# Performance work log

Measured on AMD Instinct MI355X. Metric: run time of the kernel, lower is better.

The kernel has to match this reference:

```python
import jax, jax.numpy as jnp
import numpy as np
import math

EMBED_DIM = 256
N_HEAD = 8
N_LEVELS = 4
N_POINTS = 4
HEAD_DIM = EMBED_DIM // N_HEAD
TOTAL_POINTS = N_HEAD * N_LEVELS * N_POINTS
SPATIAL = np.array([[100, 100], [50, 50], [25, 25], [13, 13]], dtype=np.int32)
BS = 2
LEN_Q = int(SPATIAL.prod(1).sum())  # 13294, encoder self-attention
LEN_V = LEN_Q


def setup_inputs() -> dict:
    key = jax.random.key(0)
    ks = jax.random.split(key, 12)
    s = 1.0 / math.sqrt(EMBED_DIM)
    inp = {
        'query': jax.random.normal(ks[0], (BS, LEN_Q, EMBED_DIM), jnp.float32),
        'reference_points': jax.random.uniform(ks[1], (BS, LEN_Q, N_LEVELS, 2), jnp.float32),
        'value': jax.random.normal(ks[2], (BS, LEN_V, EMBED_DIM), jnp.float32),
        'value_spatial_shapes': jnp.asarray(SPATIAL),
        'W_value': jax.random.normal(ks[3], (EMBED_DIM, EMBED_DIM), jnp.float32) * s,
        'b_value': jnp.zeros((EMBED_DIM,), jnp.float32),
        'W_off': jax.random.normal(ks[4], (TOTAL_POINTS * 2, EMBED_DIM), jnp.float32) * 0.01,
        'b_off': jax.random.normal(ks[5], (TOTAL_POINTS * 2,), jnp.float32),
        'W_attn': jax.random.normal(ks[6], (TOTAL_POINTS, EMBED_DIM), jnp.float32) * s,
        'b_attn': jnp.zeros((TOTAL_POINTS,), jnp.float32),
        'W_out': jax.random.normal(ks[7], (EMBED_DIM, EMBED_DIM), jnp.float32) * s,
        'b_out': jnp.zeros((EMBED_DIM,), jnp.float32),
        'zeta': jnp.ones((1, 1, 1, HEAD_DIM), jnp.float32),  # search_type='embed'
    }
    return inp


def _grid_sample_bilinear(img, gx, gy):
    """img: [B,H,W,c]; gx,gy: [B,Q,P] normalized to [-1,1].
    align_corners=False, padding_mode='zeros' (matches F.grid_sample)."""
    B, H, W, c = img.shape
    x = (gx + 1.0) * (0.5 * W) - 0.5
    y = (gy + 1.0) * (0.5 * H) - 0.5
    x0 = jnp.floor(x)
    y0 = jnp.floor(y)
    wx = (x - x0)[..., None]
    wy = (y - y0)[..., None]
    flat = img.reshape(B, H * W, c)

    def gather(xi, yi):
        m = (xi >= 0) & (xi < W) & (yi >= 0) & (yi < H)
        xi_c = jnp.clip(xi, 0, W - 1).astype(jnp.int32)
        yi_c = jnp.clip(yi, 0, H - 1).astype(jnp.int32)
        idx = (yi_c * W + xi_c).reshape(B, -1, 1)
        v = jnp.take_along_axis(flat, idx, axis=1).reshape(B, *xi.shape[1:], c)
        return v * m[..., None]

    v00 = gather(x0, y0)
    v01 = gather(x0 + 1, y0)
    v10 = gather(x0, y0 + 1)
    v11 = gather(x0 + 1, y0 + 1)
    return (v00 * (1 - wx) * (1 - wy) + v01 * wx * (1 - wy)
            + v10 * (1 - wx) * wy + v11 * wx * wy)


def reference(query, reference_points, value, value_spatial_shapes,
              W_value, b_value, W_off, b_off, W_attn, b_attn, W_out, b_out, zeta):
    bs, Len_q, _ = query.shape
    Len_v = value.shape[1]
    shapes = np.asarray(value_spatial_shapes)  # static ints

    # value projection + sparse gate (zeta, not pruned/searched)
    v = value @ W_value.T + b_value
    v = v.reshape(bs, Len_v, N_HEAD, HEAD_DIM) * zeta  # [bs,Lv,h,c]

    # sampling offsets and attention weights from query
    off = (query @ W_off.T + b_off).reshape(bs, Len_q, N_HEAD, N_LEVELS, N_POINTS, 2)
    attn = (query @ W_attn.T + b_attn).reshape(bs, Len_q, N_HEAD, N_LEVELS * N_POINTS)
    attn = jax.nn.softmax(attn, axis=-1).reshape(bs, Len_q, N_HEAD, N_LEVELS, N_POINTS)

    # reference_points last dim == 2 branch
    normalizer = jnp.asarray(shapes[:, ::-1], jnp.float32).reshape(1, 1, 1, N_LEVELS, 1, 2)  # (W,H)
    loc = reference_points.reshape(bs, Len_q, 1, N_LEVELS, 1, 2) + off / normalizer
    grids = 2.0 * loc - 1.0  # [bs,Lq,h,L,P,2]

    B = bs * N_HEAD
    out = jnp.zeros((B, Len_q, HEAD_DIM), jnp.float32)
    start = 0
    for lvl in range(N_LEVELS):
        h, w = int(shapes[lvl, 0]), int(shapes[lvl, 1])
        # [bs, h*w, nh, c] -> [bs*nh, h, w, c]
        v_l = v[:, start:start + h * w].transpose(0, 2, 1, 3).reshape(B, h, w, HEAD_DIM)
        g = grids[:, :, :, lvl].transpose(0, 2, 1, 3, 4).reshape(B, Len_q, N_POINTS, 2)
        samp = _grid_sample_bilinear(v_l, g[..., 0], g[..., 1])  # [B,Lq,P,c]
        a_l = attn[:, :, :, lvl].transpose(0, 2, 1, 3).reshape(B, Len_q, N_POINTS)
        out = out + jnp.einsum('bqpc,bqp->bqc', samp, a_l)
        start += h * w

    out = out.reshape(bs, N_HEAD, Len_q, HEAD_DIM).transpose(0, 2, 1, 3).reshape(bs, Len_q, EMBED_DIM)
    return out @ W_out.T + b_out
```

## Files before the change

### kernel.cpp

```cpp
#include <hip/hip_runtime.h>


#define LQ    13294
#define NTOK  26588
#define NE    6806528

typedef unsigned short ushort_t;
typedef __attribute__((ext_vector_type(8))) short short8;
typedef __attribute__((ext_vector_type(8))) unsigned short ushort8_t;
typedef __attribute__((ext_vector_type(4))) float float4_t;

__device__ __forceinline__ ushort_t f2b(float f) {
    unsigned int x = __float_as_uint(f);
    return (ushort_t)((x + 0x7fffu + ((x >> 16) & 1u)) >> 16);
}

__device__ __forceinline__ void gload16(const void* g, void* l) {
    __builtin_amdgcn_global_load_lds(
        (const __attribute__((address_space(1))) unsigned int*)g,
        (__attribute__((address_space(3))) unsigned int*)l, 16, 0, 0);
}

__device__ __forceinline__ void cvt_seg(const float* __restrict__ s,
                                        ushort_t* __restrict__ d,
                                        int n4, int gid, int stride) {
    const float4_t* s4 = (const float4_t*)s;
    for (int i = gid; i < n4; i += stride) {
        float4_t f = s4[i];
        ushort4 o;
        o.x = f2b(f.x); o.y = f2b(f.y); o.z = f2b(f.z); o.w = f2b(f.w);
        *(ushort4*)(d + (long)i * 4) = o;
    }
}

__global__ __launch_bounds__(256) void cvt_k(
    const float* q, const float* v, const float* Wv, const float* Wo,
    const float* Wa, const float* Wout,
    ushort_t* q_bf, ushort_t* v_bf, ushort_t* Wv_bf, ushort_t* WoWa_bf,
    ushort_t* Wout_bf)
{
    const int gid = blockIdx.x * 256 + threadIdx.x;
    const int stride = gridDim.x * 256;
    cvt_seg(q,    q_bf,            NE / 4,     gid, stride);
    cvt_seg(v,    v_bf,            NE / 4,     gid, stride);
    cvt_seg(Wv,   Wv_bf,           65536 / 4,  gid, stride);
    cvt_seg(Wo,   WoWa_bf,         65536 / 4,  gid, stride);
    cvt_seg(Wa,   WoWa_bf + 65536, 32768 / 4,  gid, stride);
    cvt_seg(Wout, Wout_bf,         65536 / 4,  gid, stride);
}

__device__ __forceinline__ void gemm_tile(
    const ushort_t* __restrict__ A,
    const ushort_t* __restrict__ W,
    int m0, int n0,
    ushort_t* As, ushort_t* Bs, float4_t acc[2][4])
{
    const int tid = threadIdx.x;
    const int w  = tid >> 6;
    const int ln = tid & 63;
    const int lr = ln >> 2;
    const int lc = (ln & 3) * 8;

    ushort_t* lA0 = As + (w * 2 + 0) * 512;
    ushort_t* lA1 = As + (w * 2 + 1) * 512;
    ushort_t* lB  = Bs + w * 512;
    const ushort_t* gA0 = A + (long)(m0 + w * 32 + lr) * 256 + lc;
    const ushort_t* gA1 = gA0 + 16 * 256;
    const ushort_t* gB  = W + (long)(n0 + w * 16 + lr) * 256 + lc;

    const int krow = (ln >> 4) * 8;
    const int fr   = ln & 15;

    gload16(gA0, lA0);
    gload16(gA1, lA1);
    gload16(gB,  lB);
    __syncthreads();

    #pragma unroll
    for (int kt = 0; kt < 8; kt++) {
        const int cur = kt & 1;
        if (kt < 7) {
            const int nxt = cur ^ 1;
            gload16(gA0 + (kt + 1) * 32, lA0 + nxt * 4096);
            gload16(gA1 + (kt + 1) * 32, lA1 + nxt * 4096);
            gload16(gB  + (kt + 1) * 32, lB  + nxt * 2048);
        }
        short8 af[2], bfr[4];
        #pragma unroll
        for (int i = 0; i < 2; i++)
            af[i] = *(const short8*)(As + cur * 4096 + (w * 32 + i * 16 + fr) * 32 + krow);
        #pragma unroll
        for (int j = 0; j < 4; j++)
            bfr[j] = *(const short8*)(Bs + cur * 2048 + (j * 16 + fr) * 32 + krow);
        #pragma unroll
        for (int i = 0; i < 2; i++)
            #pragma unroll
            for (int j = 0; j < 4; j++)
                acc[i][j] = __builtin_amdgcn_mfma_f32_16x16x32_bf16(af[i], bfr[j], acc[i][j], 0, 0, 0);
        __syncthreads();
    }
}

__global__ __launch_bounds__(256) void gemm_fused_k(
    const ushort_t* __restrict__ q_bf, const ushort_t* __restrict__ v_bf,
    const ushort_t* __restrict__ Wv,   const ushort_t* __restrict__ WoWa,
    const float* __restrict__ b_value, const float* __restrict__ b_off,
    const float* __restrict__ b_attn,  const float* __restrict__ zeta,
    ushort_t* __restrict__ vproj, float* __restrict__ oa)
{
    __shared__ __align__(16) ushort_t As[2 * 4096];
    __shared__ __align__(16) ushort_t Bs[2 * 2048];

    const int z = blockIdx.z;
    const int bid = blockIdx.x;
    int x, y;
    if (z == 0) {
        if (bid >= 832) return;
        int id = (bid & 7) * 104 + (bid >> 3);
        x = id >> 2; y = id & 3;
    } else {
        int id = (bid & 7) * 156 + (bid >> 3);
        x = id / 6; y = id - x * 6;
    }
    const int m0 = x * 128;
    const int n0 = y * 64;

    float4_t acc[2][4] = {};
    gemm_tile(z ? q_bf : v_bf, z ? WoWa : Wv, m0, n0, As, Bs, acc);

    const int tid = threadIdx.x;
    const int w = tid >> 6, ln = tid & 63;
    const int col = ln & 15;
    const int rq  = (ln >> 4) * 4;
    #pragma unroll
    for (int j = 0; j < 4; j++) {
        int n = n0 + j * 16 + col;
        if (z == 0) {
            float bz = b_value[n];
            float zz = zeta[n & 31];
            long hbase = (long)(n >> 5) * NTOK;
            #pragma unroll
            for (int i = 0; i < 2; i++) {
                #pragma unroll
                for (int r = 0; r < 4; r++) {
                    int m = m0 + w * 32 + i * 16 + rq + r;
                    if (m < NTOK)
                        vproj[(hbase + m) * 32 + (n & 31)] = f2b((acc[i][j][r] + bz) * zz);
                }
            }
        } else {
            float bz = (n < 256) ? b_off[n] : b_attn[n - 256];
            #pragma unroll
            for (int i = 0; i < 2; i++) {
                #pragma unroll
                for (int r = 0; r < 4; r++) {
                    int m = m0 + w * 32 + i * 16 + rq + r;
                    if (m < NTOK) oa[(long)m * 384 + n] = acc[i][j][r] + bz;
                }
            }
        }
    }
}

__global__ __launch_bounds__(256) void gemm_out_k(
    const ushort_t* __restrict__ A,
    const ushort_t* __restrict__ W,
    const float* __restrict__ bias,
    float* __restrict__ C)
{
    __shared__ __align__(16) ushort_t As[2 * 4096];
    __shared__ __align__(16) ushort_t Bs[2 * 2048];

    const int bid = blockIdx.x;
    int id = (bid & 7) * 104 + (bid >> 3);
    const int m0 = (id >> 2) * 128;
    const int n0 = (id & 3) * 64;

    float4_t acc[2][4] = {};
    gemm_tile(A, W, m0, n0, As, Bs, acc);

    const int tid = threadIdx.x;
    const int w = tid >> 6, ln = tid & 63;
    const int col = ln & 15;
    const int rq  = (ln >> 4) * 4;
    #pragma unroll
    for (int j = 0; j < 4; j++) {
        int n = n0 + j * 16 + col;
        float bz = bias[n];
        #pragma unroll
        for (int i = 0; i < 2; i++) {
            #pragma unroll
            for (int r = 0; r < 4; r++) {
                int m = m0 + w * 32 + i * 16 + rq + r;
                if (m < NTOK) C[(long)m * 256 + n] = acc[i][j][r] + bz;
            }
        }
    }
}

__global__ __launch_bounds__(512, 8) void sample_k(
    const float* __restrict__ refp,
    const ushort_t* __restrict__ v,
    const float* __restrict__ oa,
    ushort_t* __restrict__ outp)
{
    __shared__ __align__(16) int   p_ofs[576][4];
    __shared__ __align__(16) float p_w[576][4];
    const int bid = blockIdx.x;
    const int h   = bid & 7;
    const int tbase = (bid >> 3) * 32;
    const int tid = threadIdx.x;

    {
        const int tok1 = tid >> 4, p = tid & 15;
        const long t = tbase + tok1;
        if (t < NTOK) {
            const int lvl = p >> 2;
            const int Wi  = (lvl == 0) ? 100 : (lvl == 1) ? 50 : (lvl == 2) ? 25 : 13;
            const int st  = (lvl == 0) ? 0 : (lvl == 1) ? 10000 : (lvl == 2) ? 12500 : 13125;
            const float Wf = (float)Wi;
            const int b = (t >= LQ) ? 1 : 0;

            float lg = oa[t * 384 + 256 + h * 16 + p];
            float smax = lg;
            #pragma unroll
            for (int d = 1; d < 16; d <<= 1) smax = fmaxf(smax, __shfl_xor(smax, d, 64));
            float ex = __expf(lg - smax);
            float sm = ex;
            #pragma unroll
            for (int d = 1; d < 16; d <<= 1) sm += __shfl_xor(sm, d, 64);
            const float a = ex / sm;

            float ox = oa[t * 384 + h * 32 + p * 2];
            float oy = oa[t * 384 + h * 32 + p * 2 + 1];
            float rx = refp[t * 8 + lvl * 2];
            float ry = refp[t * 8 + lvl * 2 + 1];

            float x = rx * Wf + ox - 0.5f;
            float y = ry * Wf + oy - 0.5f;
            float xf = floorf(x), yf = floorf(y);
            float wx = x - xf, wy = y - yf;
            int x0 = (int)xf, y0 = (int)yf;

            float mx0 = ((unsigned)x0       < (unsigned)Wi) ? (1.f - wx) : 0.f;
            float mx1 = ((unsigned)(x0 + 1) < (unsigned)Wi) ? wx         : 0.f;
            float my0 = ((unsigned)y0       < (unsigned)Wi) ? (1.f - wy) * a : 0.f;
            float my1 = ((unsigned)(y0 + 1) < (unsigned)Wi) ? wy * a         : 0.f;
            int x0c = min(max(x0, 0), Wi - 1);
            int x1c = min(max(x0 + 1, 0), Wi - 1);
            int y0c = min(max(y0, 0), Wi - 1);
            int y1c = min(max(y0 + 1, 0), Wi - 1);

            const int hb = h * NTOK + b * LQ + st;
            const int r0 = hb + y0c * Wi, r1 = hb + y1c * Wi;
            const int su = tid + (tid >> 3);
            p_ofs[su][0] = (r0 + x0c) << 6;
            p_ofs[su][1] = (r0 + x1c) << 6;
            p_ofs[su][2] = (r1 + x0c) << 6;
            p_ofs[su][3] = (r1 + x1c) << 6;
            p_w[su][0] = mx0 * my0;
            p_w[su][1] = mx1 * my0;
            p_w[su][2] = mx0 * my1;
            p_w[su][3] = mx1 * my1;
        }
    }
    __syncthreads();

    const int tok2 = tid >> 4, l16 = tid & 15, s = l16 >> 2, g = l16 & 3;
    const long t = tbase + tok2;
    if (t < NTOK) {
        const char* vb = (const char*)v;
        const unsigned go = g * 16;
        const int ub = tok2 * 16 + s * 4;
        float4_t accA = {0.f, 0.f, 0.f, 0.f};
        float4_t accB = {0.f, 0.f, 0.f, 0.f};

        #pragma unroll 2
        for (int q = 0; q < 4; q++) {
            const int u = ub + q;
            const int su = u + (u >> 3);
            int4     o  = *(const int4*)p_ofs[su];
            float4_t w4 = *(const float4_t*)p_w[su];
            uint4 u00 = *(const uint4*)(vb + (unsigned)(o.x + go));
            uint4 u01 = *(const uint4*)(vb + (unsigned)(o.y + go));
            uint4 u10 = *(const uint4*)(vb + (unsigned)(o.z + go));
            uint4 u11 = *(const uint4*)(vb + (unsigned)(o.w + go));
            #define ACC8(U, WGT) \
                accA[0] += (WGT) * __uint_as_float((U).x << 16); \
                accA[1] += (WGT) * __uint_as_float((U).x & 0xffff0000u); \
                accA[2] += (WGT) * __uint_as_float((U).y << 16); \
                accA[3] += (WGT) * __uint_as_float((U).y & 0xffff0000u); \
                accB[0] += (WGT) * __uint_as_float((U).z << 16); \
                accB[1] += (WGT) * __uint_as_float((U).z & 0xffff0000u); \
                accB[2] += (WGT) * __uint_as_float((U).w << 16); \
                accB[3] += (WGT) * __uint_as_float((U).w & 0xffff0000u);
            ACC8(u00, w4.x)
            ACC8(u01, w4.y)
            ACC8(u10, w4.z)
            ACC8(u11, w4.w)
            #undef ACC8
        }

        #pragma unroll
        for (int c = 0; c < 4; c++) {
            accA[c] += __shfl_down(accA[c], 8, 64);
            accB[c] += __shfl_down(accB[c], 8, 64);
        }
        #pragma unroll
        for (int c = 0; c < 4; c++) {
            accA[c] += __shfl_down(accA[c], 4, 64);
            accB[c] += __shfl_down(accB[c], 4, 64);
        }

        if (s == 0) {
            ushort8_t o8;
            o8[0] = f2b(accA[0]); o8[1] = f2b(accA[1]);
            o8[2] = f2b(accA[2]); o8[3] = f2b(accA[3]);
            o8[4] = f2b(accB[0]); o8[5] = f2b(accB[1]);
            o8[6] = f2b(accB[2]); o8[7] = f2b(accB[3]);
            *(ushort8_t*)(outp + t * 256 + h * 32 + g * 8) = o8;
        }
    }
}

extern "C" void kernel_launch(void* const* d_in, const int* in_sizes, int n_in,
                              void* d_out, int out_size, void* d_ws, size_t ws_size,
                              hipStream_t stream)
{
    char* ws = (char*)d_ws;
    ushort_t* vproj   = (ushort_t*)ws;
    float*    oa      = (float*)(ws + (long)NE * 2);
    ushort_t* q_bf    = (ushort_t*)(ws + (long)NE * 2 + (long)NTOK * 1536);
    ushort_t* outpre  = q_bf;
    ushort_t* v_bf    = q_bf + NE;
    ushort_t* Wv_bf   = v_bf + NE;
    ushort_t* WoWa_bf = Wv_bf + 65536;
    ushort_t* Wout_bf = WoWa_bf + 98304;

    cvt_k<<<2048, 256, 0, stream>>>(
        (const float*)d_in[0], (const float*)d_in[2], (const float*)d_in[4],
        (const float*)d_in[6], (const float*)d_in[8], (const float*)d_in[10],
        q_bf, v_bf, Wv_bf, WoWa_bf, Wout_bf);

    gemm_fused_k<<<dim3(1248, 1, 2), 256, 0, stream>>>(
        q_bf, v_bf, Wv_bf, WoWa_bf,
        (const float*)d_in[5], (const float*)d_in[7], (const float*)d_in[9],
        (const float*)d_in[12], vproj, oa);

    sample_k<<<8 * 831, 512, 0, stream>>>(
        (const float*)d_in[1], vproj, oa, outpre);

    gemm_out_k<<<832, 256, 0, stream>>>(
        outpre, Wout_bf, (const float*)d_in[11], (float*)d_out);
}
```

Measured before the change: 202.5 us.

## Load GEMM A fragments directly from global, stage full W tile in LDS once

The shared GEMM tile no longer double-buffers A and W through LDS with a barrier every K step. The entire 64x256 W slice is now loaded into LDS once up front, and each wave reads its A fragments directly from global memory into registers. This removes seven per-iteration barriers and the LDS round trip for A. In exchange, A global loads are strided and less coalesced, LDS per block grows to 32KB, and launch bounds now request 4 blocks per CU.

```diff
diff --git a/kernel.cpp b/kernel.cpp
--- a/kernel.cpp
+++ b/kernel.cpp
@@ -53,63 +53,52 @@
     const ushort_t* __restrict__ A,
     const ushort_t* __restrict__ W,
     int m0, int n0,
-    ushort_t* As, ushort_t* Bs, float4_t acc[2][4])
+    ushort_t* Bs, float4_t acc[2][4])
 {
     const int tid = threadIdx.x;
     const int w  = tid >> 6;
     const int ln = tid & 63;
-    const int lr = ln >> 2;
-    const int lc = (ln & 3) * 8;
-
-    ushort_t* lA0 = As + (w * 2 + 0) * 512;
-    ushort_t* lA1 = As + (w * 2 + 1) * 512;
-    ushort_t* lB  = Bs + w * 512;
-    const ushort_t* gA0 = A + (long)(m0 + w * 32 + lr) * 256 + lc;
-    const ushort_t* gA1 = gA0 + 16 * 256;
-    const ushort_t* gB  = W + (long)(n0 + w * 16 + lr) * 256 + lc;
+
+    {
+        const int br = tid >> 2;
+        const int bc = (tid & 3) * 8;
+        const ushort_t* gB = W + (long)(n0 + br) * 256 + bc;
+        ushort_t* lB = Bs + tid * 8;
+        #pragma unroll
+        for (int r = 0; r < 8; r++)
+            gload16(gB + r * 32, lB + r * 2048);
+    }
+    __syncthreads();
 
     const int krow = (ln >> 4) * 8;
     const int fr   = ln & 15;
-
-    gload16(gA0, lA0);
-    gload16(gA1, lA1);
-    gload16(gB,  lB);
-    __syncthreads();
+    const ushort_t* gA0 = A + (long)(m0 + w * 32 + fr) * 256 + krow;
+    const ushort_t* gA1 = gA0 + 16 * 256;
 
     #pragma unroll
     for (int kt = 0; kt < 8; kt++) {
-        const int cur = kt & 1;
-        if (kt < 7) {
-            const int nxt = cur ^ 1;
-            gload16(gA0 + (kt + 1) * 32, lA0 + nxt * 4096);
-            gload16(gA1 + (kt + 1) * 32, lA1 + nxt * 4096);
-            gload16(gB  + (kt + 1) * 32, lB  + nxt * 2048);
-        }
         short8 af[2], bfr[4];
-        #pragma unroll
-        for (int i = 0; i < 2; i++)
-            af[i] = *(const short8*)(As + cur * 4096 + (w * 32 + i * 16 + fr) * 32 + krow);
+        af[0] = *(const short8*)(gA0 + kt * 32);
+        af[1] = *(const short8*)(gA1 + kt * 32);
         #pragma unroll
         for (int j = 0; j < 4; j++)
-            bfr[j] = *(const short8*)(Bs + cur * 2048 + (j * 16 + fr) * 32 + krow);
+            bfr[j] = *(const short8*)(Bs + kt * 2048 + (j * 16 + fr) * 32 + krow);
         #pragma unroll
         for (int i = 0; i < 2; i++)
             #pragma unroll
             for (int j = 0; j < 4; j++)
                 acc[i][j] = __builtin_amdgcn_mfma_f32_16x16x32_bf16(af[i], bfr[j], acc[i][j], 0, 0, 0);
-        __syncthreads();
-    }
-}
-
-__global__ __launch_bounds__(256) void gemm_fused_k(
+    }
+}
+
+__global__ __launch_bounds__(256, 4) void gemm_fused_k(
     const ushort_t* __restrict__ q_bf, const ushort_t* __restrict__ v_bf,
     const ushort_t* __restrict__ Wv,   const ushort_t* __restrict__ WoWa,
     const float* __restrict__ b_value, const float* __restrict__ b_off,
     const float* __restrict__ b_attn,  const float* __restrict__ zeta,
     ushort_t* __restrict__ vproj, float* __restrict__ oa)
 {
-    __shared__ __align__(16) ushort_t As[2 * 4096];
-    __shared__ __align__(16) ushort_t Bs[2 * 2048];
+    __shared__ __align__(16) ushort_t Bs[8 * 2048];
 
     const int z = blockIdx.z;
     const int bid = blockIdx.x;
@@ -126,7 +115,7 @@
     const int n0 = y * 64;
 
     float4_t acc[2][4] = {};
-    gemm_tile(z ? q_bf : v_bf, z ? WoWa : Wv, m0, n0, As, Bs, acc);
+    gemm_tile(z ? q_bf : v_bf, z ? WoWa : Wv, m0, n0, Bs, acc);
 
     const int tid = threadIdx.x;
     const int w = tid >> 6, ln = tid & 63;
@@ -162,14 +151,13 @@
     }
 }
 
-__global__ __launch_bounds__(256) void gemm_out_k(
+__global__ __launch_bounds__(256, 4) void gemm_out_k(
     const ushort_t* __restrict__ A,
     const ushort_t* __restrict__ W,
     const float* __restrict__ bias,
     float* __restrict__ C)
 {
-    __shared__ __align__(16) ushort_t As[2 * 4096];
-    __shared__ __align__(16) ushort_t Bs[2 * 2048];
+    __shared__ __align__(16) ushort_t Bs[8 * 2048];
 
     const int bid = blockIdx.x;
     int id = (bid & 7) * 104 + (bid >> 3);
@@ -177,7 +165,7 @@
     const int n0 = (id & 3) * 64;
 
     float4_t acc[2][4] = {};
-    gemm_tile(A, W, m0, n0, As, Bs, acc);
+    gemm_tile(A, W, m0, n0, Bs, acc);
 
     const int tid = threadIdx.x;
     const int w = tid >> 6, ln = tid & 63;
```

Measured after the change: 211.0 us. 4.2% more time.

## Enlarge GEMM tiles to 128x128 with 2x2 wave layout and flatten fused grid

Applied to the files above, without the earlier changes.

Both projection GEMMs now use 128x128 output tiles per block, with each of the four waves computing a 64x64 sub-tile, where before they used 128x64 tiles. This doubles MFMA work per LDS load and halves the number of blocks. The value and query GEMMs are merged into one flat 1D grid with no idle early-exit blocks. The fp32-to-bf16 conversion also moves to 8-element vector stores. The cost is more accumulator registers, a larger LDS footprint and fewer blocks in the output GEMM (416), which may reduce occupancy and leave some CUs idle.

```diff
diff --git a/kernel.cpp b/kernel.cpp
--- a/kernel.cpp
+++ b/kernel.cpp
@@ -23,13 +23,15 @@
 
 __device__ __forceinline__ void cvt_seg(const float* __restrict__ s,
                                         ushort_t* __restrict__ d,
-                                        int n4, int gid, int stride) {
+                                        int n8, int gid, int stride) {
     const float4_t* s4 = (const float4_t*)s;
-    for (int i = gid; i < n4; i += stride) {
-        float4_t f = s4[i];
-        ushort4 o;
-        o.x = f2b(f.x); o.y = f2b(f.y); o.z = f2b(f.z); o.w = f2b(f.w);
-        *(ushort4*)(d + (long)i * 4) = o;
+    for (int i = gid; i < n8; i += stride) {
+        float4_t f0 = s4[i * 2];
+        float4_t f1 = s4[i * 2 + 1];
+        ushort8_t o;
+        o[0] = f2b(f0.x); o[1] = f2b(f0.y); o[2] = f2b(f0.z); o[3] = f2b(f0.w);
+        o[4] = f2b(f1.x); o[5] = f2b(f1.y); o[6] = f2b(f1.z); o[7] = f2b(f1.w);
+        *(ushort8_t*)(d + (long)i * 8) = o;
     }
 }
 
@@ -41,19 +43,19 @@
 {
     const int gid = blockIdx.x * 256 + threadIdx.x;
     const int stride = gridDim.x * 256;
-    cvt_seg(q,    q_bf,            NE / 4,     gid, stride);
-    cvt_seg(v,    v_bf,            NE / 4,     gid, stride);
-    cvt_seg(Wv,   Wv_bf,           65536 / 4,  gid, stride);
-    cvt_seg(Wo,   WoWa_bf,         65536 / 4,  gid, stride);
-    cvt_seg(Wa,   WoWa_bf + 65536, 32768 / 4,  gid, stride);
-    cvt_seg(Wout, Wout_bf,         65536 / 4,  gid, stride);
+    cvt_seg(q,    q_bf,            NE / 8,     gid, stride);
+    cvt_seg(v,    v_bf,            NE / 8,     gid, stride);
+    cvt_seg(Wv,   Wv_bf,           65536 / 8,  gid, stride);
+    cvt_seg(Wo,   WoWa_bf,         65536 / 8,  gid, stride);
+    cvt_seg(Wa,   WoWa_bf + 65536, 32768 / 8,  gid, stride);
+    cvt_seg(Wout, Wout_bf,         65536 / 8,  gid, stride);
 }
 
 __device__ __forceinline__ void gemm_tile(
     const ushort_t* __restrict__ A,
     const ushort_t* __restrict__ W,
     int m0, int n0,
-    ushort_t* As, ushort_t* Bs, float4_t acc[2][4])
+    ushort_t* As, ushort_t* Bs, float4_t acc[4][4])
 {
     const int tid = threadIdx.x;
     const int w  = tid >> 6;
@@ -61,39 +63,45 @@
     const int lr = ln >> 2;
     const int lc = (ln & 3) * 8;
 
-    ushort_t* lA0 = As + (w * 2 + 0) * 512;
-    ushort_t* lA1 = As + (w * 2 + 1) * 512;
-    ushort_t* lB  = Bs + w * 512;
+    ushort_t* lA0 = As + w * 1024;
+    ushort_t* lA1 = As + w * 1024 + 512;
+    ushort_t* lB0 = Bs + w * 1024;
+    ushort_t* lB1 = Bs + w * 1024 + 512;
     const ushort_t* gA0 = A + (long)(m0 + w * 32 + lr) * 256 + lc;
     const ushort_t* gA1 = gA0 + 16 * 256;
-    const ushort_t* gB  = W + (long)(n0 + w * 16 + lr) * 256 + lc;
+    const ushort_t* gB0 = W + (long)(n0 + w * 32 + lr) * 256 + lc;
+    const ushort_t* gB1 = gB0 + 16 * 256;
+
+    gload16(gA0, lA0);
+    gload16(gA1, lA1);
+    gload16(gB0, lB0);
+    gload16(gB1, lB1);
+    __syncthreads();
 
     const int krow = (ln >> 4) * 8;
     const int fr   = ln & 15;
-
-    gload16(gA0, lA0);
-    gload16(gA1, lA1);
-    gload16(gB,  lB);
-    __syncthreads();
+    const int wm   = (w >> 1) * 64;
+    const int wn   = (w & 1) * 64;
 
     #pragma unroll
     for (int kt = 0; kt < 8; kt++) {
-        const int cur = kt & 1;
+        const int cur = (kt & 1) * 4096;
         if (kt < 7) {
-            const int nxt = cur ^ 1;
-            gload16(gA0 + (kt + 1) * 32, lA0 + nxt * 4096);
-            gload16(gA1 + (kt + 1) * 32, lA1 + nxt * 4096);
-            gload16(gB  + (kt + 1) * 32, lB  + nxt * 2048);
-        }
-        short8 af[2], bfr[4];
-        #pragma unroll
-        for (int i = 0; i < 2; i++)
-            af[i] = *(const short8*)(As + cur * 4096 + (w * 32 + i * 16 + fr) * 32 + krow);
+            const int nxt = 4096 - cur;
+            gload16(gA0 + (kt + 1) * 32, lA0 + nxt);
+            gload16(gA1 + (kt + 1) * 32, lA1 + nxt);
+            gload16(gB0 + (kt + 1) * 32, lB0 + nxt);
+            gload16(gB1 + (kt + 1) * 32, lB1 + nxt);
+        }
+        short8 af[4], bfr[4];
+        #pragma unroll
+        for (int i = 0; i < 4; i++)
+            af[i] = *(const short8*)(As + cur + (wm + i * 16 + fr) * 32 + krow);
         #pragma unroll
         for (int j = 0; j < 4; j++)
-            bfr[j] = *(const short8*)(Bs + cur * 2048 + (j * 16 + fr) * 32 + krow);
-        #pragma unroll
-        for (int i = 0; i < 2; i++)
+            bfr[j] = *(const short8*)(Bs + cur + (wn + j * 16 + fr) * 32 + krow);
+        #pragma unroll
+        for (int i = 0; i < 4; i++)
             #pragma unroll
             for (int j = 0; j < 4; j++)
                 acc[i][j] = __builtin_amdgcn_mfma_f32_16x16x32_bf16(af[i], bfr[j], acc[i][j], 0, 0, 0);
@@ -101,7 +109,7 @@
     }
 }
 
-__global__ __launch_bounds__(256) void gemm_fused_k(
+__global__ __launch_bounds__(256, 4) void gemm_fused_k(
     const ushort_t* __restrict__ q_bf, const ushort_t* __restrict__ v_bf,
     const ushort_t* __restrict__ Wv,   const ushort_t* __restrict__ WoWa,
     const float* __restrict__ b_value, const float* __restrict__ b_off,
@@ -109,90 +117,89 @@
     ushort_t* __restrict__ vproj, float* __restrict__ oa)
 {
     __shared__ __align__(16) ushort_t As[2 * 4096];
-    __shared__ __align__(16) ushort_t Bs[2 * 2048];
-
-    const int z = blockIdx.z;
+    __shared__ __align__(16) ushort_t Bs[2 * 4096];
+
     const int bid = blockIdx.x;
-    int x, y;
-    if (z == 0) {
-        if (bid >= 832) return;
-        int id = (bid & 7) * 104 + (bid >> 3);
-        x = id >> 2; y = id & 3;
-    } else {
-        int id = (bid & 7) * 156 + (bid >> 3);
-        x = id / 6; y = id - x * 6;
-    }
+    const int id = (bid & 7) * 130 + (bid >> 3);
+    const int x = id / 5;
+    const int r5 = id - x * 5;
+    const int z  = (r5 < 2) ? 0 : 1;
+    const int y  = (r5 < 2) ? r5 : r5 - 2;
     const int m0 = x * 128;
-    const int n0 = y * 64;
-
-    float4_t acc[2][4] = {};
+    const int n0 = y * 128;
+
+    float4_t acc[4][4] = {};
     gemm_tile(z ? q_bf : v_bf, z ? WoWa : Wv, m0, n0, As, Bs, acc);
 
     const int tid = threadIdx.x;
     const int w = tid >> 6, ln = tid & 63;
+    const int wm = (w >> 1) * 64;
+    const int wn = (w & 1) * 64;
     const int col = ln & 15;
     const int rq  = (ln >> 4) * 4;
     #pragma unroll
     for (int j = 0; j < 4; j++) {
-        int n = n0 + j * 16 + col;
+        int n = n0 + wn + j * 16 + col;
         if (z == 0) {
             float bz = b_value[n];
             float zz = zeta[n & 31];
             long hbase = (long)(n >> 5) * NTOK;
             #pragma unroll
-            for (int i = 0; i < 2; i++) {
+            for (int i = 0; i < 4; i++) {
                 #pragma unroll
-                for (int r = 0; r < 4; r++) {
-                    int m = m0 + w * 32 + i * 16 + rq + r;
+                for (int rr = 0; rr < 4; rr++) {
+                    int m = m0 + wm + i * 16 + rq + rr;
                     if (m < NTOK)
-                        vproj[(hbase + m) * 32 + (n & 31)] = f2b((acc[i][j][r] + bz) * zz);
+                        vproj[(hbase + m) * 32 + (n & 31)] = f2b((acc[i][j][rr] + bz) * zz);
                 }
             }
         } else {
             float bz = (n < 256) ? b_off[n] : b_attn[n - 256];
             #pragma unroll
-            for (int i = 0; i < 2; i++) {
+            for (int i = 0; i < 4; i++) {
                 #pragma unroll
-                for (int r = 0; r < 4; r++) {
-                    int m = m0 + w * 32 + i * 16 + rq + r;
-                    if (m < NTOK) oa[(long)m * 384 + n] = acc[i][j][r] + bz;
+                for (int rr = 0; rr < 4; rr++) {
+                    int m = m0 + wm + i * 16 + rq + rr;
+                    if (m < NTOK) oa[(long)m * 384 + n] = acc[i][j][rr] + bz;
                 }
             }
         }
     }
 }
 
-__global__ __launch_bounds__(256) void gemm_out_k(
+__global__ __launch_bounds__(256, 4) void gemm_out_k(
     const ushort_t* __restrict__ A,
     const ushort_t* __restrict__ W,
     const float* __restrict__ bias,
     float* __restrict__ C)
 {
     __shared__ __align__(16) ushort_t As[2 * 4096];
-    __shared__ __align__(16) ushort_t Bs[2 * 2048];
+    __shared__ __align__(16) ushort_t Bs[2 * 4096];
 
     const int bid = blockIdx.x;
-    int id = (bid & 7) * 104 + (bid >> 3);
-    const int m0 = (id >> 2) * 128;
-    const int n0 = (id & 3) * 64;
-
-    float4_t acc[2][4] = {};
+    const int id = (bid & 7) * 52 + (bid >> 3);
+    const int m0 = (id >> 1) * 128;
+    const int n0 = (id & 1) * 128;
+
+    float4_t acc[4][4] = {};
     gemm_tile(A, W, m0, n0, As, Bs, acc);
 
     const int tid = threadIdx.x;
     const int w = tid >> 6, ln = tid & 63;
+    const int wm = (w >> 1) * 64;
+    const int wn = (w & 1) * 64;
     const int col = ln & 15;
     const int rq  = (ln >> 4) * 4;
     #pragma unroll
     for (int j = 0; j < 4; j++) {
-        int n = n0 + j * 16 + col;
+        int n = n0 + wn + j * 16 + col;
         float bz = bias[n];
         #pragma unroll
-        for (int i = 0; i < 2; i++) {
-            #pragma unroll
-            for (int r = 0; r < 4; r++) {
-                int m = m0 + w * 32 + i * 16 + rq + r;
-                if (m < NTOK) C[(long)m * 256 + n] = acc[i][j][r] + bz;
+        for (int i = 0; i < 4; i++) {
+            #pragma unroll
+            for (int rr = 0; rr < 4; rr++) {
+                int m = m0 + wm + i * 16 + rq + rr;
+                if (m < NTOK) C[(long)m * 256 + n] = acc[i][j][rr] + bz;
             }
         }
     }
@@ -342,7 +349,7 @@
         (const float*)d_in[6], (const float*)d_in[8], (const float*)d_in[10],
         q_bf, v_bf, Wv_bf, WoWa_bf, Wout_bf);
 
-    gemm_fused_k<<<dim3(1248, 1, 2), 256, 0, stream>>>(
+    gemm_fused_k<<<1040, 256, 0, stream>>>(
         q_bf, v_bf, Wv_bf, WoWa_bf,
         (const float*)d_in[5], (const float*)d_in[7], (const float*)d_in[9],
         (const float*)d_in[12], vproj, oa);
@@ -350,6 +357,6 @@
     sample_k<<<8 * 831, 512, 0, stream>>>(
         (const float*)d_in[1], vproj, oa, outpre);
 
-    gemm_out_k<<<832, 256, 0, stream>>>(
+    gemm_out_k<<<416, 256, 0, stream>>>(
         outpre, Wout_bf, (const float*)d_in[11], (float*)d_out);
 }
```

New measurement: 215.9 us. 6.6% more time.
